# Kernel optimization log

Measured on AMD Instinct MI355X. Metric: run time of the kernel, lower is better.

## Reference

```python
import jax, jax.numpy as jnp
import numpy as np

N = 1 << 20          # ray samples
POS_DIM = 32         # levels * feature_dim (hash_encoding is identity stub)
DENSITY_W = 64
COLOR_W = 64


def sh4_encoding(d):
    # Fourth-order (degree-4, 16-component) real spherical harmonics, vectorized.
    x, y, z = d[..., 0], d[..., 1], d[..., 2]
    xx, yy, zz = x * x, y * y, z * z
    c0 = jnp.full_like(x, 0.28209479177387814)
    comps = [
        c0,
        0.4886025119029199 * y,
        0.4886025119029199 * z,
        0.4886025119029199 * x,
        1.0925484305920792 * x * y,
        1.0925484305920792 * y * z,
        0.9461746957575601 * zz - 0.31539156525252,
        1.0925484305920792 * x * z,
        0.5462742152960396 * (xx - yy),
        0.5900435899266435 * y * (3 * xx - yy),
        2.890611442640554 * x * y * z,
        0.4570457994644658 * y * (5 * zz - 1),
        0.3731763325901154 * z * (5 * zz - 3),
        0.4570457994644658 * x * (5 * zz - 1),
        1.445305721320277 * z * (xx - yy),
        0.5900435899266435 * x * (xx - 3 * yy),
    ]
    return jnp.stack(comps, axis=-1)  # [..., 16]


def setup_inputs() -> dict:
    key = jax.random.key(0)
    ks = jax.random.split(key, 8)
    def dense_init(k, fan_in, fan_out):
        # flax default: lecun_normal kernel, zeros bias
        w = jax.random.normal(k, (fan_in, fan_out), dtype=jnp.float32) / np.sqrt(fan_in)
        b = jnp.zeros((fan_out,), dtype=jnp.float32)
        return w, b
    position = jax.random.normal(ks[0], (N, POS_DIM), dtype=jnp.float32)
    direction = jax.random.normal(ks[1], (N, 3), dtype=jnp.float32)
    W1, b1 = dense_init(ks[2], POS_DIM, DENSITY_W)
    W2, b2 = dense_init(ks[3], DENSITY_W, 16)
    W3, b3 = dense_init(ks[4], 16 + 16, COLOR_W)
    W4, b4 = dense_init(ks[5], COLOR_W, COLOR_W)
    W5, b5 = dense_init(ks[6], COLOR_W, 3)
    return {
        "position": position, "direction": direction,
        "W1": W1, "b1": b1, "W2": W2, "b2": b2,
        "W3": W3, "b3": b3, "W4": W4, "b4": b4,
        "W5": W5, "b5": b5,
    }


def reference(position, direction, W1, b1, W2, b2, W3, b3, W4, b4, W5, b5):
    # Density MLP
    h = jax.nn.relu(position @ W1 + b1)        # [N, 64]
    density = h @ W2 + b2                      # [N, 16]
    # Color MLP on concat(density_feat, SH(dir))
    enc_dir = sh4_encoding(direction)          # [N, 16]
    c = jnp.concatenate([density, enc_dir], axis=-1)  # [N, 32]
    c = jax.nn.relu(c @ W3 + b3)               # [N, 64]
    c = jax.nn.relu(c @ W4 + b4)               # [N, 64]
    c = c @ W5 + b5                            # [N, 3]
    color = jax.nn.sigmoid(c)                  # high_dynamic_range=False
    return (density, color)
```

## Files before the change

kernel.cpp:

```cpp
#include <hip/hip_runtime.h>
#include <hip/hip_bf16.h>

typedef __bf16 bf16_t;
typedef short  s4    __attribute__((ext_vector_type(4)));
typedef float  f32x4 __attribute__((ext_vector_type(4)));

#define TPW   8
#define WAVES 4
#define ROWS_PER_BLOCK (WAVES * TPW * 16)
#define CS 36

#define FENCE() __asm__ volatile("" ::: "memory")

__device__ __forceinline__ short bfs(float f) {
    return __builtin_bit_cast(short, (bf16_t)f);
}
__device__ __forceinline__ s4 pack4(f32x4 a) {
    s4 r; r[0]=bfs(a[0]); r[1]=bfs(a[1]); r[2]=bfs(a[2]); r[3]=bfs(a[3]); return r;
}
__device__ __forceinline__ s4 relu_pack4(f32x4 a) {
    s4 r;
    r[0]=bfs(fmaxf(a[0],0.f)); r[1]=bfs(fmaxf(a[1],0.f));
    r[2]=bfs(fmaxf(a[2],0.f)); r[3]=bfs(fmaxf(a[3],0.f));
    return r;
}
#define MFMA16(a,b,c) __builtin_amdgcn_mfma_f32_16x16x16bf16_1k(a, b, c, 0, 0, 0)

__global__ __launch_bounds__(256) void nerf_fused(
    const float* __restrict__ pos, const float* __restrict__ dir,
    const float* __restrict__ W1, const float* __restrict__ b1,
    const float* __restrict__ W2, const float* __restrict__ b2,
    const float* __restrict__ W3, const float* __restrict__ b3,
    const float* __restrict__ W4, const float* __restrict__ b4,
    const float* __restrict__ W5, const float* __restrict__ b5,
    float* __restrict__ outD, float* __restrict__ outC)
{
    __shared__ float cbuf[WAVES][16 * CS];

    const int tid  = threadIdx.x;
    const int w    = tid >> 6;
    const int lane = tid & 63;
    const int q    = lane >> 4;
    const int n    = lane & 15;

    float* cb = cbuf[w];

    s4 wa1[4][2], wa2[4], wa3[4][2], wa4[4][4], wa5[4];
    #pragma unroll
    for (int t = 0; t < 4; ++t)
        #pragma unroll
        for (int kt = 0; kt < 2; ++kt)
            #pragma unroll
            for (int i = 0; i < 4; ++i)
                wa1[t][kt][i] = bfs(W1[(16*kt + 4*q + i) * 64 + 16*t + n]);
    #pragma unroll
    for (int kt = 0; kt < 4; ++kt)
        #pragma unroll
        for (int i = 0; i < 4; ++i)
            wa2[kt][i] = bfs(W2[(16*kt + 4*q + i) * 16 + n]);
    #pragma unroll
    for (int t = 0; t < 4; ++t)
        #pragma unroll
        for (int kt = 0; kt < 2; ++kt)
            #pragma unroll
            for (int i = 0; i < 4; ++i)
                wa3[t][kt][i] = bfs(W3[(16*kt + 4*q + i) * 64 + 16*t + n]);
    #pragma unroll
    for (int t = 0; t < 4; ++t)
        #pragma unroll
        for (int kt = 0; kt < 4; ++kt)
            #pragma unroll
            for (int i = 0; i < 4; ++i)
                wa4[t][kt][i] = bfs(W4[(16*kt + 4*q + i) * 64 + 16*t + n]);
    #pragma unroll
    for (int kt = 0; kt < 4; ++kt)
        #pragma unroll
        for (int i = 0; i < 4; ++i)
            wa5[kt][i] = (n < 3) ? bfs(W5[(16*kt + 4*q + i) * 3 + n]) : (short)0;

    f32x4 bi1[4], bi3[4], bi4[4], bi2, bi5;
    #pragma unroll
    for (int t = 0; t < 4; ++t)
        #pragma unroll
        for (int r = 0; r < 4; ++r) {
            bi1[t][r] = b1[16*t + 4*q + r];
            bi3[t][r] = b3[16*t + 4*q + r];
            bi4[t][r] = b4[16*t + 4*q + r];
        }
    #pragma unroll
    for (int r = 0; r < 4; ++r) {
        bi2[r] = b2[4*q + r];
        bi5[r] = (q == 0 && r < 3) ? b5[r] : 0.f;
    }

    const int waveRow0 = blockIdx.x * ROWS_PER_BLOCK + w * (TPW * 16);

    f32x4 pa = *(const f32x4*)(pos + (size_t)(waveRow0 + n) * 32 + 4*q);
    f32x4 pb = *(const f32x4*)(pos + (size_t)(waveRow0 + n) * 32 + 16 + 4*q);
    float dx = dir[(size_t)(waveRow0 + n) * 3 + 0];
    float dy = dir[(size_t)(waveRow0 + n) * 3 + 1];
    float dz = dir[(size_t)(waveRow0 + n) * 3 + 2];

    for (int t = 0; t < TPW; ++t) {
        const int row0 = waveRow0 + t * 16;
        const int rn   = waveRow0 + ((t + 1 < TPW) ? t + 1 : t) * 16;
        f32x4 pa2 = *(const f32x4*)(pos + (size_t)(rn + n) * 32 + 4*q);
        f32x4 pb2 = *(const f32x4*)(pos + (size_t)(rn + n) * 32 + 16 + 4*q);
        float dx2 = dir[(size_t)(rn + n) * 3 + 0];
        float dy2 = dir[(size_t)(rn + n) * 3 + 1];
        float dz2 = dir[(size_t)(rn + n) * 3 + 2];

        s4 xb0 = pack4(pa), xb1 = pack4(pb);

        s4 hf[4];
        #pragma unroll
        for (int tt = 0; tt < 4; ++tt) {
            f32x4 h = MFMA16(wa1[tt][0], xb0, bi1[tt]);
            h = MFMA16(wa1[tt][1], xb1, h);
            hf[tt] = relu_pack4(h);
        }

        f32x4 d2 = bi2;
        #pragma unroll
        for (int kt = 0; kt < 4; ++kt)
            d2 = MFMA16(wa2[kt], hf[kt], d2);

        *(f32x4*)(cb + n * CS + 4*q) = d2;
        FENCE();
        {
            const int rr = lane >> 2;
            const int cg = lane & 3;
            f32x4 dv = *(const f32x4*)(cb + rr * CS + 4*cg);
            *(f32x4*)(outD + (size_t)(row0 + rr) * 16 + 4*cg) = dv;
        }

        s4 cf0 = pack4(d2);
        f32x4 shv;
        {
            const float xx = dx*dx, yy = dy*dy, zz = dz*dz;
            if (q == 0) {
                shv[0] = 0.28209479177387814f;
                shv[1] = 0.4886025119029199f * dy;
                shv[2] = 0.4886025119029199f * dz;
                shv[3] = 0.4886025119029199f * dx;
            } else if (q == 1) {
                shv[0] = 1.0925484305920792f * dx * dy;
                shv[1] = 1.0925484305920792f * dy * dz;
                shv[2] = 0.9461746957575601f * zz - 0.31539156525252f;
                shv[3] = 1.0925484305920792f * dx * dz;
            } else if (q == 2) {
                shv[0] = 0.5462742152960396f * (xx - yy);
                shv[1] = 0.5900435899266435f * dy * (3.f*xx - yy);
                shv[2] = 2.890611442640554f * dx * dy * dz;
                shv[3] = 0.4570457994644658f * dy * (5.f*zz - 1.f);
            } else {
                shv[0] = 0.3731763325901154f * dz * (5.f*zz - 3.f);
                shv[1] = 0.4570457994644658f * dx * (5.f*zz - 1.f);
                shv[2] = 1.445305721320277f  * dz * (xx - yy);
                shv[3] = 0.5900435899266435f * dx * (xx - 3.f*yy);
            }
        }
        s4 cf1 = pack4(shv);

        s4 gf[4];
        #pragma unroll
        for (int tt = 0; tt < 4; ++tt) {
            f32x4 g = MFMA16(wa3[tt][0], cf0, bi3[tt]);
            g = MFMA16(wa3[tt][1], cf1, g);
            gf[tt] = relu_pack4(g);
        }

        s4 ef[4];
        #pragma unroll
        for (int tt = 0; tt < 4; ++tt) {
            f32x4 e = bi4[tt];
            #pragma unroll
            for (int kt = 0; kt < 4; ++kt)
                e = MFMA16(wa4[tt][kt], gf[kt], e);
            ef[tt] = relu_pack4(e);
        }

        f32x4 c5 = bi5;
        #pragma unroll
        for (int kt = 0; kt < 4; ++kt)
            c5 = MFMA16(wa5[kt], ef[kt], c5);
        if (q == 0) {
            f32x4 cv;
            cv[0] = 1.f / (1.f + __expf(-c5[0]));
            cv[1] = 1.f / (1.f + __expf(-c5[1]));
            cv[2] = 1.f / (1.f + __expf(-c5[2]));
            cv[3] = 0.f;
            *(f32x4*)(cb + n * CS + 32) = cv;
        }
        FENCE();
        if (lane < 48) {
            const int s = lane / 3, c = lane - 3*s;
            outC[(size_t)(row0 + s) * 3 + c] = cb[s * CS + 32 + c];
        }
        FENCE();

        pa = pa2; pb = pb2; dx = dx2; dy = dy2; dz = dz2;
    }
}

extern "C" void kernel_launch(void* const* d_in, const int* in_sizes, int n_in,
                              void* d_out, int out_size, void* d_ws, size_t ws_size,
                              hipStream_t stream) {
    const float* pos = (const float*)d_in[0];
    const float* dir = (const float*)d_in[1];
    const float* W1  = (const float*)d_in[2];
    const float* b1  = (const float*)d_in[3];
    const float* W2  = (const float*)d_in[4];
    const float* b2  = (const float*)d_in[5];
    const float* W3  = (const float*)d_in[6];
    const float* b3  = (const float*)d_in[7];
    const float* W4  = (const float*)d_in[8];
    const float* b4  = (const float*)d_in[9];
    const float* W5  = (const float*)d_in[10];
    const float* b5  = (const float*)d_in[11];

    const int N = in_sizes[0] / 32;
    float* outD = (float*)d_out;
    float* outC = outD + (size_t)N * 16;

    const int grid = N / ROWS_PER_BLOCK;
    nerf_fused<<<grid, WAVES * 64, 0, stream>>>(pos, dir, W1, b1, W2, b2, W3, b3,
                                                W4, b4, W5, b5, outD, outC);
}
```

Baseline: 277.8 us.

## Store MFMA outputs directly to global, drop LDS staging, double rows per wave

Removes the per-wave shared-memory transpose used to coalesce density and color stores. Each lane now writes its f32x4 density fragment and its three color values straight to global memory through pointers that advance each iteration. The change also doubles tiles per wave, halving the grid so weight-load setup is amortized over more rows, and adds a min-blocks launch bound. Writes become less coalesced (scattered 16B and 4B stores), and the smaller grid risks lower occupancy or tail imbalance.

```diff
diff --git a/kernel.cpp b/kernel.cpp
--- a/kernel.cpp
+++ b/kernel.cpp
@@ -5,12 +5,9 @@
 typedef short  s4    __attribute__((ext_vector_type(4)));
 typedef float  f32x4 __attribute__((ext_vector_type(4)));
 
-#define TPW   8
+#define TPW   16
 #define WAVES 4
 #define ROWS_PER_BLOCK (WAVES * TPW * 16)
-#define CS 36
-
-#define FENCE() __asm__ volatile("" ::: "memory")
 
 __device__ __forceinline__ short bfs(float f) {
     return __builtin_bit_cast(short, (bf16_t)f);
@@ -26,7 +23,7 @@
 }
 #define MFMA16(a,b,c) __builtin_amdgcn_mfma_f32_16x16x16bf16_1k(a, b, c, 0, 0, 0)
 
-__global__ __launch_bounds__(256) void nerf_fused(
+__global__ __launch_bounds__(256, 4) void nerf_fused(
     const float* __restrict__ pos, const float* __restrict__ dir,
     const float* __restrict__ W1, const float* __restrict__ b1,
     const float* __restrict__ W2, const float* __restrict__ b2,
@@ -35,16 +32,12 @@
     const float* __restrict__ W5, const float* __restrict__ b5,
     float* __restrict__ outD, float* __restrict__ outC)
 {
-    __shared__ float cbuf[WAVES][16 * CS];
-
     const int tid  = threadIdx.x;
     const int w    = tid >> 6;
     const int lane = tid & 63;
     const int q    = lane >> 4;
     const int n    = lane & 15;
 
-    float* cb = cbuf[w];
-
     s4 wa1[4][2], wa2[4], wa3[4][2], wa4[4][4], wa5[4];
     #pragma unroll
     for (int t = 0; t < 4; ++t)
@@ -95,20 +88,25 @@
 
     const int waveRow0 = blockIdx.x * ROWS_PER_BLOCK + w * (TPW * 16);
 
-    f32x4 pa = *(const f32x4*)(pos + (size_t)(waveRow0 + n) * 32 + 4*q);
-    f32x4 pb = *(const f32x4*)(pos + (size_t)(waveRow0 + n) * 32 + 16 + 4*q);
-    float dx = dir[(size_t)(waveRow0 + n) * 3 + 0];
-    float dy = dir[(size_t)(waveRow0 + n) * 3 + 1];
-    float dz = dir[(size_t)(waveRow0 + n) * 3 + 2];
+    const float* pp = pos  + (size_t)(waveRow0 + n) * 32 + 4*q;
+    const float* dp = dir  + (size_t)(waveRow0 + n) * 3;
+    float*       pD = outD + (size_t)(waveRow0 + n) * 16 + 4*q;
+    float*       pC = outC + (size_t)(waveRow0 + n) * 3;
+
+    f32x4 pa = *(const f32x4*)pp;
+    f32x4 pb = *(const f32x4*)(pp + 16);
+    float dx = dp[0];
+    float dy = dp[1];
+    float dz = dp[2];
 
     for (int t = 0; t < TPW; ++t) {
-        const int row0 = waveRow0 + t * 16;
-        const int rn   = waveRow0 + ((t + 1 < TPW) ? t + 1 : t) * 16;
-        f32x4 pa2 = *(const f32x4*)(pos + (size_t)(rn + n) * 32 + 4*q);
-        f32x4 pb2 = *(const f32x4*)(pos + (size_t)(rn + n) * 32 + 16 + 4*q);
-        float dx2 = dir[(size_t)(rn + n) * 3 + 0];
-        float dy2 = dir[(size_t)(rn + n) * 3 + 1];
-        float dz2 = dir[(size_t)(rn + n) * 3 + 2];
+        const float* ppn = pp + ((t + 1 < TPW) ? 16 * 32 : 0);
+        const float* dpn = dp + ((t + 1 < TPW) ? 16 * 3  : 0);
+        f32x4 pa2 = *(const f32x4*)ppn;
+        f32x4 pb2 = *(const f32x4*)(ppn + 16);
+        float dx2 = dpn[0];
+        float dy2 = dpn[1];
+        float dz2 = dpn[2];
 
         s4 xb0 = pack4(pa), xb1 = pack4(pb);
 
@@ -125,14 +123,7 @@
         for (int kt = 0; kt < 4; ++kt)
             d2 = MFMA16(wa2[kt], hf[kt], d2);
 
-        *(f32x4*)(cb + n * CS + 4*q) = d2;
-        FENCE();
-        {
-            const int rr = lane >> 2;
-            const int cg = lane & 3;
-            f32x4 dv = *(const f32x4*)(cb + rr * CS + 4*cg);
-            *(f32x4*)(outD + (size_t)(row0 + rr) * 16 + 4*cg) = dv;
-        }
+        *(f32x4*)pD = d2;
 
         s4 cf0 = pack4(d2);
         f32x4 shv;
@@ -184,21 +175,18 @@
         #pragma unroll
         for (int kt = 0; kt < 4; ++kt)
             c5 = MFMA16(wa5[kt], ef[kt], c5);
+
+        f32x4 cv;
+        cv[0] = 1.f / (1.f + __expf(-c5[0]));
+        cv[1] = 1.f / (1.f + __expf(-c5[1]));
+        cv[2] = 1.f / (1.f + __expf(-c5[2]));
         if (q == 0) {
-            f32x4 cv;
-            cv[0] = 1.f / (1.f + __expf(-c5[0]));
-            cv[1] = 1.f / (1.f + __expf(-c5[1]));
-            cv[2] = 1.f / (1.f + __expf(-c5[2]));
-            cv[3] = 0.f;
-            *(f32x4*)(cb + n * CS + 32) = cv;
-        }
-        FENCE();
-        if (lane < 48) {
-            const int s = lane / 3, c = lane - 3*s;
-            outC[(size_t)(row0 + s) * 3 + c] = cb[s * CS + 32 + c];
-        }
-        FENCE();
-
+            pC[0] = cv[0];
+            pC[1] = cv[1];
+            pC[2] = cv[2];
+        }
+
+        pp += 16 * 32; dp += 16 * 3; pD += 16 * 16; pC += 16 * 3;
         pa = pa2; pb = pb2; dx = dx2; dy = dy2; dz = dz2;
     }
 }
```

Result: slower. 397.0 us (+42.9%).
